# Kernel optimization log

Measured on AMD Instinct MI355X. Metric: run time of the kernel, lower is better.

## Reference

```python
import jax, jax.numpy as jnp
import numpy as np


def _maxpool2x2(x):
    # x: [N, C, H, W] -> [N, C, H//2, W//2]
    N, C, H, W = x.shape
    x = x.reshape(N, C, H // 2, 2, W // 2, 2)
    return x.max(axis=(3, 5))


def setup_inputs() -> dict:
    key = jax.random.key(0)
    ks = jax.random.split(key, 6)
    N, C, H, W = 16, 64, 64, 64
    x = jax.random.normal(ks[0], (N, C, H, W), dtype=jnp.float32)
    # 1x1 conv weights, stored as [out_ch, in_ch] (kernel is 1x1, no bias)
    w_theta = jax.random.normal(ks[1], (C >> 3, C), dtype=jnp.float32) * 0.05
    w_phi = jax.random.normal(ks[2], (C >> 3, C), dtype=jnp.float32) * 0.05
    w_g = jax.random.normal(ks[3], (C >> 1, C), dtype=jnp.float32) * 0.05
    w_o = jax.random.normal(ks[4], (C, C >> 1), dtype=jnp.float32) * 0.05
    gamma = jax.random.normal(ks[5], (), dtype=jnp.float32)
    return {"x": x, "w_theta": w_theta, "w_phi": w_phi, "w_g": w_g, "w_o": w_o, "gamma": gamma}


def reference(x, w_theta, w_phi, w_g, w_o, gamma):
    N, C, H, W = x.shape
    L = H * W           # location_num
    D = L >> 2          # downsampled_num
    # 1x1 convs as channel contractions
    theta = jnp.einsum('oc,nchw->nohw', w_theta, x).reshape(N, C >> 3, L)
    phi = _maxpool2x2(jnp.einsum('oc,nchw->nohw', w_phi, x)).reshape(N, C >> 3, D)
    attn = jax.nn.softmax(jnp.einsum('nkl,nkd->nld', theta, phi), axis=-1)  # [N, L, D]
    g = _maxpool2x2(jnp.einsum('oc,nchw->nohw', w_g, x)).reshape(N, C >> 1, D)
    attn_g = jnp.einsum('ngd,nld->ngl', g, attn).reshape(N, C >> 1, H, W)
    attn_g = jnp.einsum('og,nghw->nohw', w_o, attn_g)
    return x + gamma * attn_g
```

## Files before the change

kernel.cpp:

```cpp
#include <hip/hip_runtime.h>
#include <hip/hip_bf16.h>
#include <hip/hip_fp16.h>

#define NB 16
#define CCH 64
#define LL 4096
#define DD 1024

typedef _Float16 h8 __attribute__((ext_vector_type(8)));
typedef _Float16 h2 __attribute__((ext_vector_type(2)));
typedef float    f4v __attribute__((ext_vector_type(4)));

#if defined(__has_builtin)
#if __has_builtin(__builtin_amdgcn_fdot2)
#define HAVE_FDOT2 1
#endif
#if __has_builtin(__builtin_amdgcn_exp2f)
#define EXP2F(x) __builtin_amdgcn_exp2f(x)
#endif
#endif
#ifndef EXP2F
#define EXP2F(x) exp2f(x)
#endif

static __device__ __forceinline__ float fdot2f(h2 a, h2 b, float c) {
#ifdef HAVE_FDOT2
    return __builtin_amdgcn_fdot2(a, b, c, false);
#else
    return c + (float)a[0] * (float)b[0] + (float)a[1] * (float)b[1];
#endif
}

#define MFMA16(a, b, c) __builtin_amdgcn_mfma_f32_16x16x32_f16((a), (b), (c), 0, 0, 0)

__global__ __launch_bounds__(256, 6) void prep_kernel(
    const float* __restrict__ x,
    const float* __restrict__ w_theta,
    const float* __restrict__ w_phi,
    const float* __restrict__ w_g,
    _Float16* __restrict__ theta_out,
    _Float16* __restrict__ phi_out,
    _Float16* __restrict__ gT_out)
{
    __shared__ __align__(16) float smem[64 * 68];
    float* xs   = smem;
    float* pool = smem;

    const int n    = blockIdx.x >> 6;
    const int rem  = blockIdx.x & 63;
    const int rg   = rem >> 1;
    const int half = rem & 1;
    const int tid  = threadIdx.x;
    const int w    = tid >> 6;
    const int lane = tid & 63;
    const int m16  = lane & 15;
    const int quad = lane >> 4;

    h8 bf[3][2];
#pragma unroll
    for (int t = 0; t < 3; ++t) {
        const float* row;
        float scale = 1.0f;
        if (t == 0) {
            if (m16 < 8) { row = w_theta + m16 * 64; scale = 1.44269504f; }
            else         { row = w_phi + (m16 - 8) * 64; }
        } else if (t == 1) {
            row = w_g + m16 * 64;
        } else {
            row = w_g + (16 + m16) * 64;
        }
#pragma unroll
        for (int kc = 0; kc < 2; ++kc) {
            const float* p = row + kc * 32 + quad * 8;
            float4 a = *(const float4*)p;
            float4 b = *(const float4*)(p + 4);
            bf[t][kc][0] = (_Float16)(a.x * scale);
            bf[t][kc][1] = (_Float16)(a.y * scale);
            bf[t][kc][2] = (_Float16)(a.z * scale);
            bf[t][kc][3] = (_Float16)(a.w * scale);
            bf[t][kc][4] = (_Float16)(b.x * scale);
            bf[t][kc][5] = (_Float16)(b.y * scale);
            bf[t][kc][6] = (_Float16)(b.z * scale);
            bf[t][kc][7] = (_Float16)(b.w * scale);
        }
    }

    {
        const int ch = tid >> 2;
        const int s  = tid & 3;
        const float* xc = x + (size_t)n * CCH * LL + (size_t)ch * LL;
        float4 vv[4];
#pragma unroll
        for (int i = 0; i < 4; ++i) {
            const int f    = i * 4 + s;
            const int row  = f >> 3;
            const int colg = f & 7;
            const int l    = (rg * 2 + row) * 64 + half * 32 + colg * 4;
            vv[i] = *(const float4*)(xc + l);
        }
#pragma unroll
        for (int i = 0; i < 4; ++i) {
            const int f    = i * 4 + s;
            const int row  = f >> 3;
            const int colg = f & 7;
            *(float4*)(xs + ch * 68 + row * 32 + colg * 4) = vv[i];
        }
    }
    __syncthreads();

    h8 af[2];
#pragma unroll
    for (int kc = 0; kc < 2; ++kc) {
#pragma unroll
        for (int j = 0; j < 8; ++j) {
            float v = xs[(kc * 32 + quad * 8 + j) * 68 + w * 16 + m16];
            af[kc][j] = (_Float16)v;
        }
    }

    f4v cfr[3];
#pragma unroll
    for (int t = 0; t < 3; ++t) {
        f4v c = {0.f, 0.f, 0.f, 0.f};
        c = MFMA16(af[0], bf[t][0], c);
        c = MFMA16(af[1], bf[t][1], c);
        cfr[t] = c;
    }
    __syncthreads();

    {
#pragma unroll
        for (int t = 0; t < 3; ++t) {
#pragma unroll
            for (int r = 0; r < 4; ++r)
                pool[(w * 16 + quad * 4 + r) * 49 + t * 16 + m16] = cfr[t][r];
        }
    }
    __syncthreads();

    if (tid < 64) {
        const int px  = tid;
        const int row = px >> 5, col = px & 31;
        const int l   = (rg * 2 + row) * 64 + half * 32 + col;
        const float* pr = pool + px * 49;
        h8 tv;
#pragma unroll
        for (int k = 0; k < 8; ++k) tv[k] = (_Float16)pr[k];
        *(h8*)(theta_out + ((size_t)n * LL + l) * 8) = tv;
    }

    const int d_base = rg * 32 + half * 16;
    for (int idx = tid; idx < 640; idx += 256) {
        const int f40 = idx >> 4;
        const int pc  = idx & 15;
        const int fcol = 8 + f40;
        float v = fmaxf(fmaxf(pool[(2 * pc) * 49 + fcol],      pool[(2 * pc + 1) * 49 + fcol]),
                        fmaxf(pool[(32 + 2 * pc) * 49 + fcol], pool[(33 + 2 * pc) * 49 + fcol]));
        const int d = d_base + pc;
        if (f40 < 8) phi_out[((size_t)n * DD + d) * 8 + f40] = (_Float16)v;
        else         gT_out[((size_t)n * 32 + (f40 - 8)) * DD + d] = (_Float16)v;
    }
}

__global__ __launch_bounds__(256, 8) void attn_kernel(
    const float*    __restrict__ x,
    const _Float16* __restrict__ theta,
    const _Float16* __restrict__ phi,
    const _Float16* __restrict__ gT,
    const float*    __restrict__ w_o,
    const float*    __restrict__ gamma_p,
    float*          __restrict__ out)
{
    __shared__ __align__(16) char smem[18944 + 512];
    _Float16* phi_s  = (_Float16*)smem;
    float*    red    = (float*)smem;
    float*    out_s  = (float*)smem;
    float*    ssum_s = (float*)(smem + 18944);

    const int n    = blockIdx.x >> 7;
    const int lblk = blockIdx.x & 127;
    const int tid  = threadIdx.x;
    const int h    = tid >> 6;
    const int lane = tid & 63;
    const int m16  = lane & 15;
    const int quad = lane >> 4;
    const int l0   = lblk * 32;

    const _Float16* gT_n = gT + (size_t)n * 32 * DD;

    {
        const float4* ps = (const float4*)(phi + (size_t)n * DD * 8);
        float4* pd = (float4*)phi_s;
#pragma unroll
        for (int i = 0; i < 4; ++i) {
            const int d = tid + 256 * i;
            pd[d + (d >> 3)] = ps[d];
        }
    }

    h8 th0 = *(const h8*)(theta + ((size_t)n * LL + l0 + m16) * 8);
    h8 th1 = *(const h8*)(theta + ((size_t)n * LL + l0 + 16 + m16) * 8);
    const h2* t0p = (const h2*)&th0;
    const h2* t1p = (const h2*)&th1;

    const int vp = h >> 1;
    h8 wof[2];
#pragma unroll
    for (int i = 0; i < 2; ++i) {
        const float* wr = w_o + (size_t)(m16 + 16 * (vp * 2 + i)) * 32 + quad * 8;
        float4 wa = *(const float4*)wr;
        float4 wb = *(const float4*)(wr + 4);
        wof[i][0] = (_Float16)wa.x; wof[i][1] = (_Float16)wa.y;
        wof[i][2] = (_Float16)wa.z; wof[i][3] = (_Float16)wa.w;
        wof[i][4] = (_Float16)wb.x; wof[i][5] = (_Float16)wb.y;
        wof[i][6] = (_Float16)wb.z; wof[i][7] = (_Float16)wb.w;
    }

    __syncthreads();

    f4v c00 = {0.f, 0.f, 0.f, 0.f}, c01 = c00, c10 = c00, c11 = c00;
    float ssum0 = 0.f, ssum1 = 0.f;

    const _Float16* gr0 = gT_n + (size_t)m16 * DD + h * 256 + quad * 8;
    const _Float16* gr1 = gT_n + (size_t)(16 + m16) * DD + h * 256 + quad * 8;
    const int pb = h * 256 + quad * 8;
    const _Float16* pr = phi_s + (size_t)(pb + (pb >> 3)) * 8;

#pragma unroll 2
    for (int c = 0; c < 8; ++c) {
        const int d0 = c * 32;
        h8 b0 = *(const h8*)(gr0 + d0);
        h8 b1 = *(const h8*)(gr1 + d0);
        const _Float16* prc = pr + c * 288;
        h8 a0, a1;
#pragma unroll
        for (int j = 0; j < 8; ++j) {
            h8 ph = *(const h8*)(prc + j * 8);
            const h2* pp = (const h2*)&ph;
            float u0 = fdot2f(t0p[0], pp[0], 0.f);
            u0 = fdot2f(t0p[1], pp[1], u0);
            float v0 = fdot2f(t0p[2], pp[2], 0.f);
            v0 = fdot2f(t0p[3], pp[3], v0);
            float u1 = fdot2f(t1p[0], pp[0], 0.f);
            u1 = fdot2f(t1p[1], pp[1], u1);
            float v1 = fdot2f(t1p[2], pp[2], 0.f);
            v1 = fdot2f(t1p[3], pp[3], v1);
            float e0 = EXP2F(u0 + v0);
            float e1 = EXP2F(u1 + v1);
            ssum0 += e0; ssum1 += e1;
            a0[j] = (_Float16)e0;
            a1[j] = (_Float16)e1;
        }
        c00 = MFMA16(a0, b0, c00);
        c01 = MFMA16(a0, b1, c01);
        c10 = MFMA16(a1, b0, c10);
        c11 = MFMA16(a1, b1, c11);
    }

    ssum0 += __shfl_xor(ssum0, 16); ssum0 += __shfl_xor(ssum0, 32);
    ssum1 += __shfl_xor(ssum1, 16); ssum1 += __shfl_xor(ssum1, 32);
    if (quad == 0) {
        ssum_s[h * 32 + m16]      = ssum0;
        ssum_s[h * 32 + 16 + m16] = ssum1;
    }
    __syncthreads();

    {
        float* rg = red + (size_t)h * 32 * 37;
#pragma unroll
        for (int r = 0; r < 4; ++r) {
            const int rr = quad * 4 + r;
            rg[rr * 37 + m16]             = c00[r];
            rg[rr * 37 + 16 + m16]        = c01[r];
            rg[(16 + rr) * 37 + m16]      = c10[r];
            rg[(16 + rr) * 37 + 16 + m16] = c11[r];
        }
    }
    __syncthreads();

    const int t = h & 1;
    h8 pa;
    {
        const int q = t * 16 + m16;
        const float* rq = red + q * 37 + quad * 8;
        float ss = ssum_s[q] + ssum_s[32 + q] + ssum_s[64 + q] + ssum_s[96 + q];
        float inv = 1.0f / ss;
#pragma unroll
        for (int j = 0; j < 8; ++j) {
            float sv = rq[j] + rq[32 * 37 + j] + rq[64 * 37 + j] + rq[96 * 37 + j];
            pa[j] = (_Float16)(sv * inv);
        }
    }
    __syncthreads();

    const f4v zero = {0.f, 0.f, 0.f, 0.f};
#pragma unroll
    for (int i = 0; i < 2; ++i) {
        f4v pv = MFMA16(pa, wof[i], zero);
        const int och = m16 + 16 * (vp * 2 + i);
        float* od = out_s + (size_t)(t * 16 + quad * 4) * 68 + och;
#pragma unroll
        for (int r = 0; r < 4; ++r) od[r * 68] = pv[r];
    }
    __syncthreads();

    const float gamma = gamma_p[0];
    const int soch = tid >> 2;
    const int qoff = (tid & 3) * 8;
    const float* xrow = x   + (size_t)n * CCH * LL + (size_t)soch * LL + l0 + qoff;
    float*       orow = out + (size_t)n * CCH * LL + (size_t)soch * LL + l0 + qoff;
#pragma unroll
    for (int i = 0; i < 2; ++i) {
        float4 xv = *(const float4*)(xrow + i * 4);
        float4 ov;
        ov.x = xv.x + gamma * out_s[(qoff + i * 4)     * 68 + soch];
        ov.y = xv.y + gamma * out_s[(qoff + i * 4 + 1) * 68 + soch];
        ov.z = xv.z + gamma * out_s[(qoff + i * 4 + 2) * 68 + soch];
        ov.w = xv.w + gamma * out_s[(qoff + i * 4 + 3) * 68 + soch];
        *(float4*)(orow + i * 4) = ov;
    }
}

extern "C" void kernel_launch(void* const* d_in, const int* in_sizes, int n_in,
                              void* d_out, int out_size, void* d_ws, size_t ws_size,
                              hipStream_t stream) {
    const float* x       = (const float*)d_in[0];
    const float* w_theta = (const float*)d_in[1];
    const float* w_phi   = (const float*)d_in[2];
    const float* w_g     = (const float*)d_in[3];
    const float* w_o     = (const float*)d_in[4];
    const float* gamma   = (const float*)d_in[5];
    float* out = (float*)d_out;

    _Float16* theta_h = (_Float16*)d_ws;
    _Float16* phi_h   = theta_h + (size_t)NB * LL * 8;
    _Float16* gT_h    = phi_h   + (size_t)NB * DD * 8;

    prep_kernel<<<1024, 256, 0, stream>>>(x, w_theta, w_phi, w_g,
                                          theta_h, phi_h, gT_h);
    attn_kernel<<<2048, 256, 0, stream>>>(x, theta_h, phi_h, gT_h,
                                          w_o, gamma, out);
}
```

Baseline: 113.1 us.

## Compute attention scores with MFMA instead of fdot2 loops

Replaces the per-lane fdot2 score computation (theta·phi over 8 channels) with MFMA 16x16x32 instructions. The K dimension is zero-padded from 8 to 32 by only letting quad 0 supply data. The MFMA output layout is remapped so that the exp results feed the next MFMA directly, and the gT loads are split into two h4 halves to match the permuted D ordering. The phi shared-memory padding is removed because the access pattern changed. The cost is wasted MFMA work on zero-padded K and extra MFMA latency per chunk, in exchange for far fewer VALU dot instructions.

```diff
diff --git a/kernel.cpp b/kernel.cpp
--- a/kernel.cpp
+++ b/kernel.cpp
@@ -8,13 +8,11 @@
 #define DD 1024
 
 typedef _Float16 h8 __attribute__((ext_vector_type(8)));
+typedef _Float16 h4 __attribute__((ext_vector_type(4)));
 typedef _Float16 h2 __attribute__((ext_vector_type(2)));
 typedef float    f4v __attribute__((ext_vector_type(4)));
 
 #if defined(__has_builtin)
-#if __has_builtin(__builtin_amdgcn_fdot2)
-#define HAVE_FDOT2 1
-#endif
 #if __has_builtin(__builtin_amdgcn_exp2f)
 #define EXP2F(x) __builtin_amdgcn_exp2f(x)
 #endif
@@ -22,14 +20,6 @@
 #ifndef EXP2F
 #define EXP2F(x) exp2f(x)
 #endif
-
-static __device__ __forceinline__ float fdot2f(h2 a, h2 b, float c) {
-#ifdef HAVE_FDOT2
-    return __builtin_amdgcn_fdot2(a, b, c, false);
-#else
-    return c + (float)a[0] * (float)b[0] + (float)a[1] * (float)b[1];
-#endif
-}
 
 #define MFMA16(a, b, c) __builtin_amdgcn_mfma_f32_16x16x32_f16((a), (b), (c), 0, 0, 0)
 
@@ -194,14 +184,16 @@
 #pragma unroll
         for (int i = 0; i < 4; ++i) {
             const int d = tid + 256 * i;
-            pd[d + (d >> 3)] = ps[d];
+            pd[d] = ps[d];
         }
     }
 
     h8 th0 = *(const h8*)(theta + ((size_t)n * LL + l0 + m16) * 8);
     h8 th1 = *(const h8*)(theta + ((size_t)n * LL + l0 + 16 + m16) * 8);
-    const h2* t0p = (const h2*)&th0;
-    const h2* t1p = (const h2*)&th1;
+
+    const h8 zero8 = {};
+    h8 bq0 = (quad == 0) ? th0 : zero8;
+    h8 bq1 = (quad == 0) ? th1 : zero8;
 
     const int vp = h >> 1;
     h8 wof[2];
@@ -221,36 +213,47 @@
     f4v c00 = {0.f, 0.f, 0.f, 0.f}, c01 = c00, c10 = c00, c11 = c00;
     float ssum0 = 0.f, ssum1 = 0.f;
 
-    const _Float16* gr0 = gT_n + (size_t)m16 * DD + h * 256 + quad * 8;
-    const _Float16* gr1 = gT_n + (size_t)(16 + m16) * DD + h * 256 + quad * 8;
-    const int pb = h * 256 + quad * 8;
-    const _Float16* pr = phi_s + (size_t)(pb + (pb >> 3)) * 8;
+    const _Float16* gq0 = gT_n + (size_t)m16 * DD + h * 256;
+    const _Float16* gq1 = gT_n + (size_t)(16 + m16) * DD + h * 256;
+    const _Float16* ph_base = phi_s + (size_t)(h * 256 + m16) * 8;
 
 #pragma unroll 2
     for (int c = 0; c < 8; ++c) {
         const int d0 = c * 32;
-        h8 b0 = *(const h8*)(gr0 + d0);
-        h8 b1 = *(const h8*)(gr1 + d0);
-        const _Float16* prc = pr + c * 288;
-        h8 a0, a1;
-#pragma unroll
-        for (int j = 0; j < 8; ++j) {
-            h8 ph = *(const h8*)(prc + j * 8);
-            const h2* pp = (const h2*)&ph;
-            float u0 = fdot2f(t0p[0], pp[0], 0.f);
-            u0 = fdot2f(t0p[1], pp[1], u0);
-            float v0 = fdot2f(t0p[2], pp[2], 0.f);
-            v0 = fdot2f(t0p[3], pp[3], v0);
-            float u1 = fdot2f(t1p[0], pp[0], 0.f);
-            u1 = fdot2f(t1p[1], pp[1], u1);
-            float v1 = fdot2f(t1p[2], pp[2], 0.f);
-            v1 = fdot2f(t1p[3], pp[3], v1);
-            float e0 = EXP2F(u0 + v0);
-            float e1 = EXP2F(u1 + v1);
-            ssum0 += e0; ssum1 += e1;
-            a0[j] = (_Float16)e0;
-            a1[j] = (_Float16)e1;
-        }
+
+        h8 ap0 = zero8, ap1 = zero8;
+        if (quad == 0) {
+            ap0 = *(const h8*)(ph_base + d0 * 8);
+            ap1 = *(const h8*)(ph_base + (d0 + 16) * 8);
+        }
+
+        h4 b0lo = *(const h4*)(gq0 + d0 + quad * 4);
+        h4 b0hi = *(const h4*)(gq0 + d0 + 16 + quad * 4);
+        h4 b1lo = *(const h4*)(gq1 + d0 + quad * 4);
+        h4 b1hi = *(const h4*)(gq1 + d0 + 16 + quad * 4);
+        h8 b0 = __builtin_shufflevector(b0lo, b0hi, 0, 1, 2, 3, 4, 5, 6, 7);
+        h8 b1 = __builtin_shufflevector(b1lo, b1hi, 0, 1, 2, 3, 4, 5, 6, 7);
+
+        const f4v z4 = {0.f, 0.f, 0.f, 0.f};
+
+        f4v s00 = MFMA16(ap0, bq0, z4);
+        f4v s10 = MFMA16(ap1, bq0, z4);
+        h8 a0;
+#pragma unroll
+        for (int r = 0; r < 4; ++r) {
+            float e0 = EXP2F(s00[r]); ssum0 += e0; a0[r]     = (_Float16)e0;
+            float f0 = EXP2F(s10[r]); ssum0 += f0; a0[4 + r] = (_Float16)f0;
+        }
+
+        f4v s01 = MFMA16(ap0, bq1, z4);
+        f4v s11 = MFMA16(ap1, bq1, z4);
+        h8 a1;
+#pragma unroll
+        for (int r = 0; r < 4; ++r) {
+            float e1 = EXP2F(s01[r]); ssum1 += e1; a1[r]     = (_Float16)e1;
+            float f1 = EXP2F(s11[r]); ssum1 += f1; a1[4 + r] = (_Float16)f1;
+        }
+
         c00 = MFMA16(a0, b0, c00);
         c01 = MFMA16(a0, b1, c01);
         c10 = MFMA16(a1, b0, c10);
```

After: 130.3 us. +15.3%, slower.
